# Performance work log

Hardware: AMD Instinct MI355X
Metric: run time of the kernel (lower is better)

The kernel has to match this reference:

```python
import jax, jax.numpy as jnp
import numpy as np

N = 150000   # nodes
E = 150000   # edges per edge type
D = 128      # n_map
T = 10       # edge types: pre0-3, suc0-3, left, right
L = 4        # fuse layers
VOCAB = 16   # mark_type_dim
EPS = 1e-5


def _mlp(x, W1, b1, W2, b2):
    # MLPLayer(in, hid, out): Linear -> ReLU -> Linear
    return jax.nn.relu(x @ W1.T + b1) @ W2.T + b2


def setup_inputs() -> dict:
    key = jax.random.key(0)
    ks = iter(jax.random.split(key, 40))
    s = 0.02
    f = lambda shape: (jax.random.normal(next(ks), shape, dtype=jnp.float32) * s)
    inp = {
        'ctrs': jax.random.normal(next(ks), (N, 2), dtype=jnp.float32),
        'feats': jax.random.normal(next(ks), (N, 2), dtype=jnp.float32),
        # input MLP (2 -> D -> D)
        'in_W1': f((D, 2)), 'in_b1': f((D,)), 'in_W2': f((D, D)), 'in_b2': f((D,)),
        # seg MLP (2 -> D -> D)
        'seg_W1': f((D, 2)), 'seg_b1': f((D,)), 'seg_W2': f((D, D)), 'seg_b2': f((D,)),
        # mark embedding and meta MLP (2D -> D -> D)
        'embed': f((VOCAB, D)),
        'meta_W1': f((D, 2 * D)), 'meta_b1': f((D,)), 'meta_W2': f((D, D)), 'meta_b2': f((D,)),
        # fuse weights stacked over L layers
        'ctr_W': f((L, D, D)),            # Linear no bias
        'edge_W': f((L, T, D, D)),        # per-edge-type Linear no bias
        'norm_g': jnp.ones((L, D), jnp.float32),
        'norm_b': jnp.zeros((L, D), jnp.float32),
        'ctr2_W1': f((L, D, D)), 'ctr2_b1': f((L, D)),
        'ctr2_W2': f((L, D, D)), 'ctr2_b2': f((L, D)),
        # integer graph structure
        'mark_type': jax.random.randint(next(ks), (N,), 0, VOCAB, dtype=jnp.int32),
        'edge_u': jax.random.randint(next(ks), (T, E), 0, N, dtype=jnp.int32),
        'edge_v': jax.random.randint(next(ks), (T, E), 0, N, dtype=jnp.int32),
    }
    return inp


def reference(ctrs, feats, in_W1, in_b1, in_W2, in_b2,
              seg_W1, seg_b1, seg_W2, seg_b2,
              embed, meta_W1, meta_b1, meta_W2, meta_b2,
              ctr_W, edge_W, norm_g, norm_b,
              ctr2_W1, ctr2_b1, ctr2_W2, ctr2_b2,
              mark_type, edge_u, edge_v):
    feat = jax.nn.relu(_mlp(ctrs, in_W1, in_b1, in_W2, in_b2)
                       + _mlp(feats, seg_W1, seg_b1, seg_W2, seg_b2))  # [N, D]
    res = feat
    for i in range(L):
        temp = feat @ ctr_W[i].T
        for t in range(T):  # gather -> small GEMM -> scatter-add per edge type
            msg = feat[edge_v[t]] @ edge_W[i, t].T        # [E, D]
            temp = temp.at[edge_u[t]].add(msg)
        # GroupNorm(1, D) on [N, D]: normalize over channels per node
        mu = jnp.mean(temp, axis=-1, keepdims=True)
        var = jnp.var(temp, axis=-1, keepdims=True)
        feat = (temp - mu) * jax.lax.rsqrt(var + EPS) * norm_g[i] + norm_b[i]
        feat = jax.nn.relu(feat)
        feat = _mlp(feat, ctr2_W1[i], ctr2_b1[i], ctr2_W2[i], ctr2_b2[i])
        feat = jax.nn.relu(feat + res)
        res = feat
    meta = embed[mark_type]                               # [N, D]
    feat = _mlp(jnp.concatenate([feat, meta], axis=1), meta_W1, meta_b1, meta_W2, meta_b2)
    return feat
```

## Files before the change

kernel.cpp:

```cpp
#include <hip/hip_runtime.h>

#define D 128
#define NT 10
#define NL 4
#define BN 128
#define SCH 1024

typedef __attribute__((ext_vector_type(8))) short bf16x8;
typedef __attribute__((ext_vector_type(4))) float f32x4;

__device__ inline unsigned short f2bf(float x) {
    union { float f; unsigned u; } v; v.f = x;
    unsigned r = v.u + 0x7FFFu + ((v.u >> 16) & 1u);
    return (unsigned short)(r >> 16);
}
__device__ inline float bf2f(unsigned short h) {
    union { unsigned u; float f; } v; v.u = ((unsigned)h) << 16;
    return v.f;
}

__global__ void input_hidden_kernel(const float* __restrict__ ctrs,
                                    const float* __restrict__ feats,
                                    const float* __restrict__ inW1,
                                    const float* __restrict__ inb1,
                                    const float* __restrict__ segW1,
                                    const float* __restrict__ segb1,
                                    float* __restrict__ h_in,
                                    float* __restrict__ h_seg, int N) {
    int gid = blockIdx.x * blockDim.x + threadIdx.x;
    int n = gid >> 5;
    int c = gid & 31;
    if (n >= N) return;
    float x0 = ctrs[2 * n], x1 = ctrs[2 * n + 1];
    float y0 = feats[2 * n], y1 = feats[2 * n + 1];
    int o0 = c * 4;
    float hi[4], hs[4];
#pragma unroll
    for (int j = 0; j < 4; ++j) {
        int o = o0 + j;
        float a = fmaf(x0, inW1[2 * o], fmaf(x1, inW1[2 * o + 1], inb1[o]));
        hi[j] = fmaxf(a, 0.f);
        float b = fmaf(y0, segW1[2 * o], fmaf(y1, segW1[2 * o + 1], segb1[o]));
        hs[j] = fmaxf(b, 0.f);
    }
    *(float4*)&h_in[(size_t)n * D + o0] = make_float4(hi[0], hi[1], hi[2], hi[3]);
    *(float4*)&h_seg[(size_t)n * D + o0] = make_float4(hs[0], hs[1], hs[2], hs[3]);
}

template <int BIAS, int RELU, int ADDIN>
__global__ __launch_bounds__(256) void gemm_mfma_kernel(
    const float* __restrict__ A, const float* __restrict__ W,
    const float* __restrict__ bias, const float* addin, float* out, int N,
    int ldw) {
    __shared__ unsigned short a_hi[128][40], a_lo[128][40];
    __shared__ unsigned short w_hi[128][40], w_lo[128][40];
    int t = threadIdx.x;
    int wave = t >> 6, lane = t & 63;
    int fr = lane & 15, fq = lane >> 4;
    int n0 = blockIdx.x * BN;
    f32x4 acc[2][8];
#pragma unroll
    for (int m = 0; m < 2; ++m)
#pragma unroll
        for (int n = 0; n < 8; ++n) acc[m][n] = (f32x4){0.f, 0.f, 0.f, 0.f};

    for (int kc = 0; kc < 4; ++kc) {
        int k0 = kc * 32;
#pragma unroll
        for (int i = 0; i < 4; ++i) {
            int idx = i * 256 + t;
            int row = idx >> 3, c4 = idx & 7;
            int n = n0 + row;
            float4 v = make_float4(0.f, 0.f, 0.f, 0.f);
            if (n < N) v = *(const float4*)&A[(size_t)n * D + k0 + c4 * 4];
            ushort4 h, l;
            h.x = f2bf(v.x); l.x = f2bf(v.x - bf2f(h.x));
            h.y = f2bf(v.y); l.y = f2bf(v.y - bf2f(h.y));
            h.z = f2bf(v.z); l.z = f2bf(v.z - bf2f(h.z));
            h.w = f2bf(v.w); l.w = f2bf(v.w - bf2f(h.w));
            *(ushort4*)&a_hi[row][c4 * 4] = h;
            *(ushort4*)&a_lo[row][c4 * 4] = l;
        }
#pragma unroll
        for (int i = 0; i < 4; ++i) {
            int idx = i * 256 + t;
            int row = idx >> 3, c4 = idx & 7;
            float4 v = *(const float4*)&W[(size_t)row * ldw + k0 + c4 * 4];
            ushort4 h, l;
            h.x = f2bf(v.x); l.x = f2bf(v.x - bf2f(h.x));
            h.y = f2bf(v.y); l.y = f2bf(v.y - bf2f(h.y));
            h.z = f2bf(v.z); l.z = f2bf(v.z - bf2f(h.z));
            h.w = f2bf(v.w); l.w = f2bf(v.w - bf2f(h.w));
            *(ushort4*)&w_hi[row][c4 * 4] = h;
            *(ushort4*)&w_lo[row][c4 * 4] = l;
        }
        __syncthreads();

        bf16x8 ah[2], al[2];
#pragma unroll
        for (int m = 0; m < 2; ++m) {
            int row = wave * 32 + m * 16 + fr;
            ah[m] = *(const bf16x8*)&a_hi[row][fq * 8];
            al[m] = *(const bf16x8*)&a_lo[row][fq * 8];
        }
#pragma unroll
        for (int n = 0; n < 8; ++n) {
            int wr = n * 16 + fr;
            bf16x8 wh = *(const bf16x8*)&w_hi[wr][fq * 8];
            bf16x8 wl = *(const bf16x8*)&w_lo[wr][fq * 8];
#pragma unroll
            for (int m = 0; m < 2; ++m) {
                acc[m][n] = __builtin_amdgcn_mfma_f32_16x16x32_bf16(
                    ah[m], wh, acc[m][n], 0, 0, 0);
                acc[m][n] = __builtin_amdgcn_mfma_f32_16x16x32_bf16(
                    ah[m], wl, acc[m][n], 0, 0, 0);
                acc[m][n] = __builtin_amdgcn_mfma_f32_16x16x32_bf16(
                    al[m], wh, acc[m][n], 0, 0, 0);
            }
        }
        __syncthreads();
    }
#pragma unroll
    for (int m = 0; m < 2; ++m) {
#pragma unroll
        for (int j = 0; j < 4; ++j) {
            int row = n0 + wave * 32 + m * 16 + fq * 4 + j;
            if (row < N) {
#pragma unroll
                for (int n = 0; n < 8; ++n) {
                    int col = n * 16 + fr;
                    float r = acc[m][n][j];
                    if (BIAS) r += bias[col];
                    if (ADDIN) r += addin[(size_t)row * D + col];
                    if (RELU) r = fmaxf(r, 0.f);
                    out[(size_t)row * D + col] = r;
                }
            }
        }
    }
}

__global__ void scatter_add_kernel(const float* __restrict__ Y,
                                   const int* __restrict__ eu,
                                   const int* __restrict__ ev, float* temp,
                                   int E) {
    int gid = blockIdx.x * blockDim.x + threadIdx.x;
    int e = gid >> 5;
    int c = gid & 31;
    if (e >= E) return;
    int u = eu[e], v = ev[e];
    float4 m = *(const float4*)&Y[(size_t)v * D + c * 4];
    float* dst = &temp[(size_t)u * D + c * 4];
    unsafeAtomicAdd(dst + 0, m.x);
    unsafeAtomicAdd(dst + 1, m.y);
    unsafeAtomicAdd(dst + 2, m.z);
    unsafeAtomicAdd(dst + 3, m.w);
}

__global__ void csr_hist_kernel(const int* __restrict__ edge_u, int* deg,
                                int N, int E) {
    int gid = blockIdx.x * blockDim.x + threadIdx.x;
    if (gid >= NT * E) return;
    int t = gid / E;
    int u = edge_u[gid];
    atomicAdd(&deg[(size_t)t * N + u], 1);
}

__global__ __launch_bounds__(256) void csr_chunksum_kernel(
    const int* __restrict__ deg, int* csum, int N, int nch) {
    int b = blockIdx.x;
    int t = b / nch, ch = b % nch;
    int tid = threadIdx.x;
    const int* dg = deg + (size_t)t * N;
    int base = ch * SCH + tid * 4;
    int s = 0;
#pragma unroll
    for (int j = 0; j < 4; ++j) {
        int idx = base + j;
        if (idx < N) s += dg[idx];
    }
#pragma unroll
    for (int off = 32; off; off >>= 1) s += __shfl_down(s, off);
    __shared__ int wsum[4];
    if ((tid & 63) == 0) wsum[tid >> 6] = s;
    __syncthreads();
    if (tid == 0) csum[b] = wsum[0] + wsum[1] + wsum[2] + wsum[3];
}

__global__ void csr_chunkscan_kernel(int* csum, int* rowptr, int N, int nch) {
    int t = threadIdx.x;
    if (t >= NT) return;
    int run = 0;
    for (int i = 0; i < nch; ++i) {
        int v = csum[t * nch + i];
        csum[t * nch + i] = run;
        run += v;
    }
    rowptr[(size_t)t * (N + 1) + N] = run;
}

__global__ __launch_bounds__(256) void csr_blockscan_kernel(
    const int* __restrict__ deg, const int* __restrict__ csum, int* rowptr,
    int* cur, int N, int nch) {
    int b = blockIdx.x;
    int t = b / nch, ch = b % nch;
    int tid = threadIdx.x;
    const int* dg = deg + (size_t)t * N;
    int base = ch * SCH + tid * 4;
    int d[4];
    int s = 0;
#pragma unroll
    for (int j = 0; j < 4; ++j) {
        int idx = base + j;
        d[j] = (idx < N) ? dg[idx] : 0;
        s += d[j];
    }
    __shared__ int ps[256];
    ps[tid] = s;
    __syncthreads();
    for (int off = 1; off < 256; off <<= 1) {
        int v = (tid >= off) ? ps[tid - off] : 0;
        __syncthreads();
        ps[tid] += v;
        __syncthreads();
    }
    int excl = (tid ? ps[tid - 1] : 0) + csum[b];
    size_t rb = (size_t)t * (N + 1);
#pragma unroll
    for (int j = 0; j < 4; ++j) {
        int idx = base + j;
        if (idx < N) {
            rowptr[rb + idx] = excl;
            cur[rb + idx] = excl;
            excl += d[j];
        }
    }
}

__global__ void csr_fill_kernel(const int* __restrict__ edge_u,
                                const int* __restrict__ edge_v, int* cur,
                                int* col, int N, int E) {
    int gid = blockIdx.x * blockDim.x + threadIdx.x;
    if (gid >= NT * E) return;
    int t = gid / E;
    int u = edge_u[gid];
    int v = edge_v[gid];
    int pos = atomicAdd(&cur[(size_t)t * (N + 1) + u], 1);
    col[(size_t)t * E + pos] = v;
}

__global__ __launch_bounds__(256) void csr_gather_kernel(
    const float* __restrict__ Y, const int* __restrict__ rowptr,
    const int* __restrict__ col, float* temp, int N) {
    int wid = (int)((blockIdx.x * (size_t)blockDim.x + threadIdx.x) >> 6);
    int lane = threadIdx.x & 63;
    if (wid >= N) return;
    int beg = rowptr[wid];
    int end = rowptr[wid + 1];
    if (beg == end) return;
    size_t ro = (size_t)wid * D + lane * 2;
    float2 acc = *(float2*)&temp[ro];
    for (int k = beg; k < end; ++k) {
        int v = col[k];
        float2 y = *(const float2*)&Y[(size_t)v * D + lane * 2];
        acc.x += y.x;
        acc.y += y.y;
    }
    *(float2*)&temp[ro] = acc;
}

__global__ __launch_bounds__(256) void norm_relu_kernel(float* temp,
                                                        const float* __restrict__ g,
                                                        const float* __restrict__ b,
                                                        int N) {
    int wid = (int)((blockIdx.x * (size_t)blockDim.x + threadIdx.x) >> 6);
    int lane = threadIdx.x & 63;
    if (wid >= N) return;
    float2 x = *(float2*)&temp[(size_t)wid * D + lane * 2];
    float s = x.x + x.y;
    float sq = x.x * x.x + x.y * x.y;
#pragma unroll
    for (int off = 32; off; off >>= 1) {
        s += __shfl_xor(s, off);
        sq += __shfl_xor(sq, off);
    }
    float mu = s * (1.f / 128.f);
    float var = sq * (1.f / 128.f) - mu * mu;
    float rs = rsqrtf(var + 1e-5f);
    float r0 = fmaxf(fmaf((x.x - mu) * rs, g[lane * 2], b[lane * 2]), 0.f);
    float r1 = fmaxf(fmaf((x.y - mu) * rs, g[lane * 2 + 1], b[lane * 2 + 1]), 0.f);
    *(float2*)&temp[(size_t)wid * D + lane * 2] = make_float2(r0, r1);
}

__global__ void gather_meta_kernel(const int* __restrict__ mark,
                                   const float* __restrict__ embed, float* out,
                                   int N) {
    int gid = blockIdx.x * blockDim.x + threadIdx.x;
    int n = gid >> 5;
    int c = gid & 31;
    if (n >= N) return;
    *(float4*)&out[(size_t)n * D + c * 4] =
        *(const float4*)&embed[(size_t)mark[n] * D + c * 4];
}

static inline void launch_gemm(const float* A, const float* W, const float* bias,
                               const float* addin, float* out, int N, int ldw,
                               bool relu, hipStream_t s) {
    dim3 grid((N + BN - 1) / BN), blk(256);
    bool B = bias != nullptr, AD = addin != nullptr;
    if (B && !relu && !AD)
        gemm_mfma_kernel<1, 0, 0><<<grid, blk, 0, s>>>(A, W, bias, addin, out, N, ldw);
    else if (B && relu && AD)
        gemm_mfma_kernel<1, 1, 1><<<grid, blk, 0, s>>>(A, W, bias, addin, out, N, ldw);
    else if (!B && !relu && !AD)
        gemm_mfma_kernel<0, 0, 0><<<grid, blk, 0, s>>>(A, W, bias, addin, out, N, ldw);
    else if (B && relu && !AD)
        gemm_mfma_kernel<1, 1, 0><<<grid, blk, 0, s>>>(A, W, bias, addin, out, N, ldw);
    else if (!B && relu && AD)
        gemm_mfma_kernel<0, 1, 1><<<grid, blk, 0, s>>>(A, W, bias, addin, out, N, ldw);
    else if (!B && relu && !AD)
        gemm_mfma_kernel<0, 1, 0><<<grid, blk, 0, s>>>(A, W, bias, addin, out, N, ldw);
    else if (!B && !relu && AD)
        gemm_mfma_kernel<0, 0, 1><<<grid, blk, 0, s>>>(A, W, bias, addin, out, N, ldw);
    else
        gemm_mfma_kernel<1, 0, 1><<<grid, blk, 0, s>>>(A, W, bias, addin, out, N, ldw);
}

extern "C" void kernel_launch(void* const* d_in, const int* in_sizes, int n_in,
                              void* d_out, int out_size, void* d_ws,
                              size_t ws_size, hipStream_t stream) {
    const float* ctrs = (const float*)d_in[0];
    const float* feats = (const float*)d_in[1];
    const float* in_W1 = (const float*)d_in[2];
    const float* in_b1 = (const float*)d_in[3];
    const float* in_W2 = (const float*)d_in[4];
    const float* in_b2 = (const float*)d_in[5];
    const float* seg_W1 = (const float*)d_in[6];
    const float* seg_b1 = (const float*)d_in[7];
    const float* seg_W2 = (const float*)d_in[8];
    const float* seg_b2 = (const float*)d_in[9];
    const float* embed = (const float*)d_in[10];
    const float* meta_W1 = (const float*)d_in[11];
    const float* meta_b1 = (const float*)d_in[12];
    const float* meta_W2 = (const float*)d_in[13];
    const float* meta_b2 = (const float*)d_in[14];
    const float* ctr_W = (const float*)d_in[15];
    const float* edge_W = (const float*)d_in[16];
    const float* norm_g = (const float*)d_in[17];
    const float* norm_b = (const float*)d_in[18];
    const float* ctr2_W1 = (const float*)d_in[19];
    const float* ctr2_b1 = (const float*)d_in[20];
    const float* ctr2_W2 = (const float*)d_in[21];
    const float* ctr2_b2 = (const float*)d_in[22];
    const int* mark_type = (const int*)d_in[23];
    const int* edge_u = (const int*)d_in[24];
    const int* edge_v = (const int*)d_in[25];

    const int N = in_sizes[0] / 2;
    const int E = in_sizes[24] / NT;
    const size_t ND = (size_t)N * D;
    const int nch = (N + SCH - 1) / SCH;

    float* F = (float*)d_ws;
    float* T1 = (float*)d_ws + ND;
    float* SC = (float*)d_out;

    int* rowptr = (int*)((float*)d_ws + 2 * ND);
    int* col = rowptr + (size_t)NT * (N + 1);
    size_t ws_need = (2 * ND) * sizeof(float) +
                     ((size_t)NT * (N + 1) + (size_t)NT * E) * sizeof(int);
    size_t out_need = ((size_t)NT * N + (size_t)NT * (N + 1) +
                       2 * (size_t)NT * nch) * sizeof(int);
    bool use_csr = (ws_size >= ws_need) &&
                   ((size_t)out_size * sizeof(float) >= out_need);

    dim3 blk(256);
    dim3 g32((N * 32 + 255) / 256);
    dim3 g64(((size_t)N * 64 + 255) / 256);
    dim3 gE((E * 32 + 255) / 256);
    dim3 gTE(((size_t)NT * E + 255) / 256);

    if (use_csr) {
        int* deg = (int*)d_out;
        int* cur = deg + (size_t)NT * N;
        int* csum = cur + (size_t)NT * (N + 1);
        hipMemsetAsync(deg, 0, (size_t)NT * N * sizeof(int), stream);
        csr_hist_kernel<<<gTE, blk, 0, stream>>>(edge_u, deg, N, E);
        csr_chunksum_kernel<<<NT * nch, blk, 0, stream>>>(deg, csum, N, nch);
        csr_chunkscan_kernel<<<1, 64, 0, stream>>>(csum, rowptr, N, nch);
        csr_blockscan_kernel<<<NT * nch, blk, 0, stream>>>(deg, csum, rowptr,
                                                           cur, N, nch);
        csr_fill_kernel<<<gTE, blk, 0, stream>>>(edge_u, edge_v, cur, col, N, E);
    }

    input_hidden_kernel<<<g32, blk, 0, stream>>>(ctrs, feats, in_W1, in_b1,
                                                 seg_W1, seg_b1, T1, SC, N);
    launch_gemm(T1, in_W2, in_b2, nullptr, F, N, D, false, stream);
    launch_gemm(SC, seg_W2, seg_b2, F, F, N, D, true, stream);

    for (int i = 0; i < NL; ++i) {
        launch_gemm(F, ctr_W + (size_t)i * D * D, nullptr, nullptr, T1, N, D,
                    false, stream);
        for (int t = 0; t < NT; ++t) {
            launch_gemm(F, edge_W + ((size_t)i * NT + t) * D * D, nullptr,
                        nullptr, SC, N, D, false, stream);
            if (use_csr) {
                csr_gather_kernel<<<g64, blk, 0, stream>>>(
                    SC, rowptr + (size_t)t * (N + 1), col + (size_t)t * E, T1, N);
            } else {
                scatter_add_kernel<<<gE, blk, 0, stream>>>(
                    SC, edge_u + (size_t)t * E, edge_v + (size_t)t * E, T1, E);
            }
        }
        norm_relu_kernel<<<g64, blk, 0, stream>>>(T1, norm_g + (size_t)i * D,
                                                  norm_b + (size_t)i * D, N);
        launch_gemm(T1, ctr2_W1 + (size_t)i * D * D, ctr2_b1 + (size_t)i * D,
                    nullptr, SC, N, D, true, stream);
        launch_gemm(SC, ctr2_W2 + (size_t)i * D * D, ctr2_b2 + (size_t)i * D, F,
                    F, N, D, true, stream);
    }

    gather_meta_kernel<<<g32, blk, 0, stream>>>(mark_type, embed, SC, N);
    launch_gemm(F, meta_W1, meta_b1, nullptr, T1, N, 2 * D, false, stream);
    launch_gemm(SC, meta_W1 + D, nullptr, T1, T1, N, 2 * D, true, stream);
    launch_gemm(T1, meta_W2, meta_b2, nullptr, (float*)d_out, N, D, false,
                stream);
}
```

Before: 4.004 ms.

## Batch edge-type GEMM outputs in workspace and gather multiple types per pass

Computes the per-edge-type transformed features into several workspace slots, then runs a single CSR gather over all buffered edge types at once. This saves repeated read-modify-write passes over the accumulator. When every type fits in one group, GroupNorm and ReLU are fused into that gather, removing the separate norm pass. Whether it applies depends on workspace size; otherwise it falls back to the per-type path. The atomic scatter fallback is removed, so the non-CSR configuration no longer has a valid path.

```diff
diff --git a/kernel.cpp b/kernel.cpp
--- a/kernel.cpp
+++ b/kernel.cpp
@@ -140,23 +140,6 @@
     }
 }
 
-__global__ void scatter_add_kernel(const float* __restrict__ Y,
-                                   const int* __restrict__ eu,
-                                   const int* __restrict__ ev, float* temp,
-                                   int E) {
-    int gid = blockIdx.x * blockDim.x + threadIdx.x;
-    int e = gid >> 5;
-    int c = gid & 31;
-    if (e >= E) return;
-    int u = eu[e], v = ev[e];
-    float4 m = *(const float4*)&Y[(size_t)v * D + c * 4];
-    float* dst = &temp[(size_t)u * D + c * 4];
-    unsafeAtomicAdd(dst + 0, m.x);
-    unsafeAtomicAdd(dst + 1, m.y);
-    unsafeAtomicAdd(dst + 2, m.z);
-    unsafeAtomicAdd(dst + 3, m.w);
-}
-
 __global__ void csr_hist_kernel(const int* __restrict__ edge_u, int* deg,
                                 int N, int E) {
     int gid = blockIdx.x * blockDim.x + threadIdx.x;
@@ -249,22 +232,42 @@
     col[(size_t)t * E + pos] = v;
 }
 
-__global__ __launch_bounds__(256) void csr_gather_kernel(
+template <int NORM>
+__global__ __launch_bounds__(256) void csr_gather_multi_kernel(
     const float* __restrict__ Y, const int* __restrict__ rowptr,
-    const int* __restrict__ col, float* temp, int N) {
+    const int* __restrict__ col, float* temp, int N, int nt, size_t strideY,
+    int E, const float* __restrict__ g, const float* __restrict__ b) {
     int wid = (int)((blockIdx.x * (size_t)blockDim.x + threadIdx.x) >> 6);
     int lane = threadIdx.x & 63;
     if (wid >= N) return;
-    int beg = rowptr[wid];
-    int end = rowptr[wid + 1];
-    if (beg == end) return;
     size_t ro = (size_t)wid * D + lane * 2;
     float2 acc = *(float2*)&temp[ro];
-    for (int k = beg; k < end; ++k) {
-        int v = col[k];
-        float2 y = *(const float2*)&Y[(size_t)v * D + lane * 2];
-        acc.x += y.x;
-        acc.y += y.y;
+    for (int j = 0; j < nt; ++j) {
+        const int* rp = rowptr + (size_t)j * (N + 1);
+        int beg = rp[wid];
+        int end = rp[wid + 1];
+        const float* Yj = Y + (size_t)j * strideY;
+        const int* cj = col + (size_t)j * E;
+        for (int k = beg; k < end; ++k) {
+            int v = cj[k];
+            float2 y = *(const float2*)&Yj[(size_t)v * D + lane * 2];
+            acc.x += y.x;
+            acc.y += y.y;
+        }
+    }
+    if (NORM) {
+        float s = acc.x + acc.y;
+        float sq = acc.x * acc.x + acc.y * acc.y;
+#pragma unroll
+        for (int off = 32; off; off >>= 1) {
+            s += __shfl_xor(s, off);
+            sq += __shfl_xor(sq, off);
+        }
+        float mu = s * (1.f / 128.f);
+        float var = sq * (1.f / 128.f) - mu * mu;
+        float rs = rsqrtf(var + 1e-5f);
+        acc.x = fmaxf(fmaf((acc.x - mu) * rs, g[lane * 2], b[lane * 2]), 0.f);
+        acc.y = fmaxf(fmaf((acc.y - mu) * rs, g[lane * 2 + 1], b[lane * 2 + 1]), 0.f);
     }
     *(float2*)&temp[ro] = acc;
 }
@@ -367,17 +370,22 @@
 
     int* rowptr = (int*)((float*)d_ws + 2 * ND);
     int* col = rowptr + (size_t)NT * (N + 1);
-    size_t ws_need = (2 * ND) * sizeof(float) +
+    size_t base_ws = (2 * ND) * sizeof(float) +
                      ((size_t)NT * (N + 1) + (size_t)NT * E) * sizeof(int);
     size_t out_need = ((size_t)NT * N + (size_t)NT * (N + 1) +
                        2 * (size_t)NT * nch) * sizeof(int);
-    bool use_csr = (ws_size >= ws_need) &&
+    bool use_csr = (ws_size >= base_ws) &&
                    ((size_t)out_size * sizeof(float) >= out_need);
+
+    float* Yws = (float*)((char*)d_ws + ((base_ws + 255) & ~(size_t)255));
+    int slots = 0;
+    if (use_csr && ws_size > base_ws + 256)
+        slots = (int)((ws_size - base_ws - 256) / (ND * sizeof(float)));
+    if (slots > NT) slots = NT;
 
     dim3 blk(256);
     dim3 g32((N * 32 + 255) / 256);
     dim3 g64(((size_t)N * 64 + 255) / 256);
-    dim3 gE((E * 32 + 255) / 256);
     dim3 gTE(((size_t)NT * E + 255) / 256);
 
     if (use_csr) {
@@ -401,19 +409,39 @@
     for (int i = 0; i < NL; ++i) {
         launch_gemm(F, ctr_W + (size_t)i * D * D, nullptr, nullptr, T1, N, D,
                     false, stream);
-        for (int t = 0; t < NT; ++t) {
-            launch_gemm(F, edge_W + ((size_t)i * NT + t) * D * D, nullptr,
-                        nullptr, SC, N, D, false, stream);
-            if (use_csr) {
-                csr_gather_kernel<<<g64, blk, 0, stream>>>(
-                    SC, rowptr + (size_t)t * (N + 1), col + (size_t)t * E, T1, N);
-            } else {
-                scatter_add_kernel<<<gE, blk, 0, stream>>>(
-                    SC, edge_u + (size_t)t * E, edge_v + (size_t)t * E, T1, E);
+        if (use_csr && slots >= 1) {
+            int ngroups = (NT + slots - 1) / slots;
+            for (int g0 = 0, grp = 0; g0 < NT; g0 += slots, ++grp) {
+                int nt = (NT - g0 < slots) ? (NT - g0) : slots;
+                for (int j = 0; j < nt; ++j)
+                    launch_gemm(F, edge_W + ((size_t)i * NT + g0 + j) * D * D,
+                                nullptr, nullptr, Yws + (size_t)j * ND, N, D,
+                                false, stream);
+                bool last = (grp == ngroups - 1);
+                if (last && ngroups == 1)
+                    csr_gather_multi_kernel<1><<<g64, blk, 0, stream>>>(
+                        Yws, rowptr + (size_t)g0 * (N + 1), col + (size_t)g0 * E,
+                        T1, N, nt, ND, E, norm_g + (size_t)i * D,
+                        norm_b + (size_t)i * D);
+                else
+                    csr_gather_multi_kernel<0><<<g64, blk, 0, stream>>>(
+                        Yws, rowptr + (size_t)g0 * (N + 1), col + (size_t)g0 * E,
+                        T1, N, nt, ND, E, nullptr, nullptr);
             }
-        }
-        norm_relu_kernel<<<g64, blk, 0, stream>>>(T1, norm_g + (size_t)i * D,
-                                                  norm_b + (size_t)i * D, N);
+            if (ngroups > 1)
+                norm_relu_kernel<<<g64, blk, 0, stream>>>(
+                    T1, norm_g + (size_t)i * D, norm_b + (size_t)i * D, N);
+        } else {
+            for (int t = 0; t < NT; ++t) {
+                launch_gemm(F, edge_W + ((size_t)i * NT + t) * D * D, nullptr,
+                            nullptr, SC, N, D, false, stream);
+                csr_gather_multi_kernel<0><<<g64, blk, 0, stream>>>(
+                    SC, rowptr + (size_t)t * (N + 1), col + (size_t)t * E, T1,
+                    N, 1, 0, E, nullptr, nullptr);
+            }
+            norm_relu_kernel<<<g64, blk, 0, stream>>>(
+                T1, norm_g + (size_t)i * D, norm_b + (size_t)i * D, N);
+        }
         launch_gemm(T1, ctr2_W1 + (size_t)i * D * D, ctr2_b1 + (size_t)i * D,
                     nullptr, SC, N, D, true, stream);
         launch_gemm(SC, ctr2_W2 + (size_t)i * D * D, ctr2_b2 + (size_t)i * D, F,
```

Result: slower. 4.722 ms (+17.9%).
